# Performance work log

Hardware: AMD Instinct MI355X
Metric: run time of the kernel (lower is better)

Reference implementation:

```python
import jax, jax.numpy as jnp
import numpy as np

B, T, H, D = 4, 2048, 16, 128
ATTN = H * D
FREQ_BASE = 10000.0


def _rope(t, base):
    # t: [B, T, H, D]; ggml-style interleaved RoPE on pairs (2i, 2i+1)
    d = t.shape[-1]
    seq = t.shape[1]
    pos = jnp.arange(seq, dtype=jnp.float32)                      # [T]
    inv_freq = base ** (-jnp.arange(0, d, 2, dtype=jnp.float32) / d)  # [D/2]
    ang = pos[:, None] * inv_freq[None, :]                        # [T, D/2]
    cos = jnp.cos(ang)[None, :, None, :]                          # [1,T,1,D/2]
    sin = jnp.sin(ang)[None, :, None, :]
    t1 = t[..., 0::2]
    t2 = t[..., 1::2]
    r1 = t1 * cos - t2 * sin
    r2 = t1 * sin + t2 * cos
    return jnp.stack([r1, r2], axis=-1).reshape(t.shape)


def setup_inputs() -> dict:
    key = jax.random.key(0)
    ks = jax.random.split(key, 12)
    s = 1.0 / np.sqrt(ATTN)
    return {
        "x": jax.random.normal(ks[0], (B, T, ATTN), dtype=jnp.float32),
        "freqs_cos": jax.random.normal(ks[1], (T, D // 2), dtype=jnp.float32),
        "freqs_sin": jax.random.normal(ks[2], (T, D // 2), dtype=jnp.float32),
        "wq_w": jax.random.normal(ks[3], (ATTN, ATTN), dtype=jnp.float32) * s,
        "wq_b": jax.random.normal(ks[4], (ATTN,), dtype=jnp.float32) * s,
        "wk_w": jax.random.normal(ks[5], (ATTN, ATTN), dtype=jnp.float32) * s,
        "wk_b": jax.random.normal(ks[6], (ATTN,), dtype=jnp.float32) * s,
        "wv_w": jax.random.normal(ks[7], (ATTN, ATTN), dtype=jnp.float32) * s,
        "wv_b": jax.random.normal(ks[8], (ATTN,), dtype=jnp.float32) * s,
        "wo_w": jax.random.normal(ks[9], (ATTN, ATTN), dtype=jnp.float32) * s,
        "wo_b": jax.random.normal(ks[10], (ATTN,), dtype=jnp.float32) * s,
    }


def reference(x, freqs_cos, freqs_sin, wq_w, wq_b, wk_w, wk_b, wv_w, wv_b, wo_w, wo_b):
    # freqs_cos / freqs_sin accepted for signature compatibility but ignored
    b, t, _ = x.shape
    q = (x @ wq_w.T + wq_b).reshape(b, t, H, D)
    k = (x @ wk_w.T + wk_b).reshape(b, t, H, D)
    v = (x @ wv_w.T + wv_b).reshape(b, t, H, D)
    q = _rope(q, FREQ_BASE)
    k = _rope(k, FREQ_BASE)
    # causal SDPA over [B, H, T, D]
    scale = 1.0 / np.sqrt(D).astype(np.float32)
    scores = jnp.einsum("bqhd,bkhd->bhqk", q, k) * scale          # [B,H,T,T]
    mask = jnp.tril(jnp.ones((t, t), dtype=bool))
    scores = jnp.where(mask[None, None], scores, jnp.finfo(scores.dtype).min)
    probs = jax.nn.softmax(scores, axis=-1)
    y = jnp.einsum("bhqk,bkhd->bqhd", probs, v).reshape(b, t, H * D)
    return y @ wo_w.T + wo_b
```

## Files before the change

### kernel.cpp

```cpp
#include <hip/hip_runtime.h>
#include <math.h>

#define Tt 2048
#define Hh 16
#define Dd 128
#define ATTN 2048

typedef unsigned short u16;
typedef __attribute__((ext_vector_type(8))) short short8;
typedef __attribute__((ext_vector_type(4))) float f32x4;

__device__ __forceinline__ float bf2f(u16 h) {
    union { unsigned int u; float f; } x;
    x.u = ((unsigned int)h) << 16;
    return x.f;
}
__device__ __forceinline__ u16 f2bf(float f) {
    union { float f; unsigned int u; } x;
    x.f = f;
    unsigned int r = x.u + 0x7fffu + ((x.u >> 16) & 1u);
    return (u16)(r >> 16);
}
__device__ __forceinline__ void gl_lds16(const void* g, void* l) {
    __builtin_amdgcn_global_load_lds(
        (const __attribute__((address_space(1))) unsigned int*)g,
        (__attribute__((address_space(3))) unsigned int*)l, 16, 0, 0);
}

__global__ __launch_bounds__(256) void freq_kernel(float* __restrict__ cost,
                                                   float* __restrict__ sint) {
    int idx = blockIdx.x * 256 + threadIdx.x;
    if (idx >= Tt * 64) return;
    int t = idx >> 6, i = idx & 63;
    double inv = exp(-((double)(2 * i) / 128.0) * log(10000.0));
    double ang = (double)t * inv;
    cost[idx] = (float)cos(ang);
    sint[idx] = (float)sin(ang);
}

__global__ __launch_bounds__(256) void cvt_kernel(const float* __restrict__ in,
                                                  u16* __restrict__ out, int n4) {
    int i = blockIdx.x * 256 + threadIdx.x;
    if (i >= n4) return;
    float4 v = *(const float4*)(in + (size_t)i * 4);
    union { ushort4 u; u16 s[4]; } pk;
    pk.s[0] = f2bf(v.x); pk.s[1] = f2bf(v.y);
    pk.s[2] = f2bf(v.z); pk.s[3] = f2bf(v.w);
    *(ushort4*)(out + (size_t)i * 4) = pk.u;
}

template<int MODE>
__global__ __launch_bounds__(512, 2) void gemm_mfma(const u16* __restrict__ A,
                                                    const u16* __restrict__ W,
                                                    const float* __restrict__ bias,
                                                    void* __restrict__ Cout) {
    extern __shared__ u16 lds[];
    const int tid  = threadIdx.x;
    const int lane = tid & 63, w = tid >> 6;
    const int l15  = lane & 15, quad = lane >> 4;
    const int wm = w >> 2, wn = w & 3;

    const int id = blockIdx.x;
    const int bx = id & 7, by = id >> 3;
    const int m0 = by * 256, n0 = bx * 256;

    const f32x4 zero4 = {0.f, 0.f, 0.f, 0.f};
    f32x4 acc[8][4];
#pragma unroll
    for (int mt = 0; mt < 8; mt++)
#pragma unroll
        for (int nt = 0; nt < 4; nt++) acc[mt][nt] = zero4;

    const int srow = w * 16 + (lane >> 3);
    const int gsc  = ((lane & 7) ^ (lane >> 3)) * 8;
    const u16* Ag = A + (size_t)(m0 + srow) * 2048 + gsc;
    const u16* Wg = W + (size_t)(n0 + srow) * 2048 + gsc;
    const int wB = w * 1024;

    const int s7 = l15 & 7;
    const int cA = wm * 8192 + l15 * 64;
    const int cB = 16384 + (wn >> 1) * 8192 + ((wn & 1) * 64 + l15) * 64;
    const int ck0 = (quad ^ s7) * 8;
    const int ck1 = ((quad ^ s7) ^ 4) * 8;

#define STAGE(tt, dd, ss) do { \
    const u16* _g = (((ss) < 2) ? Ag : Wg) + (((ss) & 1) ? (size_t)(128 * 2048) : (size_t)0) \
                    + (size_t)(tt) * 64; \
    u16* _l = lds + (dd) * 32768 + (ss) * 8192 + wB; \
    gl_lds16(_g, _l); \
    gl_lds16(_g + (size_t)8 * 2048, _l + 512); \
} while (0)

    STAGE(0, 0, 0); STAGE(0, 0, 1); STAGE(0, 0, 2); STAGE(0, 0, 3);
    STAGE(1, 1, 0); STAGE(1, 1, 1);

    short8 af[4][2], bf[4][2];
    for (int t = 0; t < 32; t++) {
        const int d = t & 1, e = d ^ 1;
        const u16* bufd = lds + d * 32768;

        if (t < 31) { asm volatile("s_waitcnt vmcnt(4)" ::: "memory"); }
        else        { asm volatile("s_waitcnt vmcnt(0)" ::: "memory"); }
        __builtin_amdgcn_sched_barrier(0);
        __builtin_amdgcn_s_barrier();
        __builtin_amdgcn_sched_barrier(0);

#pragma unroll
        for (int mt = 0; mt < 4; mt++) {
            af[mt][0] = *(const short8*)(bufd + cA + mt * 1024 + ck0);
            af[mt][1] = *(const short8*)(bufd + cA + mt * 1024 + ck1);
        }
#pragma unroll
        for (int nt = 0; nt < 4; nt++) {
            bf[nt][0] = *(const short8*)(bufd + cB + nt * 1024 + ck0);
            bf[nt][1] = *(const short8*)(bufd + cB + nt * 1024 + ck1);
        }
        if (t + 1 < 32) STAGE(t + 1, e, 2);
        if (t + 1 < 32) STAGE(t + 1, e, 3);
        __builtin_amdgcn_s_setprio(1);
#pragma unroll
        for (int mt = 0; mt < 4; mt++)
#pragma unroll
            for (int nt = 0; nt < 4; nt++) {
                acc[mt][nt] = __builtin_amdgcn_mfma_f32_16x16x32_bf16(
                    af[mt][0], bf[nt][0], acc[mt][nt], 0, 0, 0);
                acc[mt][nt] = __builtin_amdgcn_mfma_f32_16x16x32_bf16(
                    af[mt][1], bf[nt][1], acc[mt][nt], 0, 0, 0);
            }
        __builtin_amdgcn_s_setprio(0);
#pragma unroll
        for (int mt = 0; mt < 4; mt++) {
            af[mt][0] = *(const short8*)(bufd + cA + (mt + 4) * 1024 + ck0);
            af[mt][1] = *(const short8*)(bufd + cA + (mt + 4) * 1024 + ck1);
        }
        asm volatile("s_waitcnt lgkmcnt(0)" ::: "memory");
        __builtin_amdgcn_sched_barrier(0);
        __builtin_amdgcn_s_barrier();
        __builtin_amdgcn_sched_barrier(0);
        if (t + 2 < 32) { STAGE(t + 2, d, 0); STAGE(t + 2, d, 1); }
        __builtin_amdgcn_s_setprio(1);
#pragma unroll
        for (int mt = 0; mt < 4; mt++)
#pragma unroll
            for (int nt = 0; nt < 4; nt++) {
                acc[mt + 4][nt] = __builtin_amdgcn_mfma_f32_16x16x32_bf16(
                    af[mt][0], bf[nt][0], acc[mt + 4][nt], 0, 0, 0);
                acc[mt + 4][nt] = __builtin_amdgcn_mfma_f32_16x16x32_bf16(
                    af[mt][1], bf[nt][1], acc[mt + 4][nt], 0, 0, 0);
            }
        __builtin_amdgcn_s_setprio(0);
    }
#undef STAGE

    float bn[4];
#pragma unroll
    for (int nt = 0; nt < 4; nt++) bn[nt] = bias[n0 + wn * 64 + nt * 16 + l15];

    if (MODE == 0) {
        float* C = (float*)Cout;
#pragma unroll
        for (int mt = 0; mt < 8; mt++) {
            int m = m0 + wm * 128 + mt * 16 + quad * 4;
#pragma unroll
            for (int nt = 0; nt < 4; nt++) {
                int n = n0 + wn * 64 + nt * 16 + l15;
#pragma unroll
                for (int r = 0; r < 4; r++)
                    C[(size_t)(m + r) * 2048 + n] = acc[mt][nt][r] + bn[nt];
            }
        }
    } else if (MODE == 1) {
        u16* C = (u16*)Cout;
#pragma unroll
        for (int mt = 0; mt < 8; mt++) {
            int m = m0 + wm * 128 + mt * 16 + quad * 4;
            int b = m >> 11, tr = m & 2047;
#pragma unroll
            for (int nt = 0; nt < 4; nt++) {
                int n = n0 + wn * 64 + nt * 16 + l15;
                int h = n >> 7, dd = n & 127;
                size_t base = ((size_t)(b * Hh + h) * Tt + tr) * Dd + dd;
#pragma unroll
                for (int r = 0; r < 4; r++)
                    C[base + (size_t)r * Dd] = f2bf(acc[mt][nt][r] + bn[nt]);
            }
        }
    } else {
        u16* C = (u16*)Cout;
        const int b = m0 >> 11;
#pragma unroll
        for (int mt = 0; mt < 8; mt++) {
            int tloc = (m0 & 2047) + wm * 128 + mt * 16 + quad * 4;
#pragma unroll
            for (int nt = 0; nt < 4; nt++) {
                int n = n0 + wn * 64 + nt * 16 + l15;
                int h = n >> 7, dd = n & 127;
                union { ushort4 u; u16 s[4]; } pk;
#pragma unroll
                for (int r = 0; r < 4; r++) pk.s[r] = f2bf(acc[mt][nt][r] + bn[nt]);
                *(ushort4*)&C[((size_t)(b * Hh + h) * Dd + dd) * Tt + tloc] = pk.u;
            }
        }
    }
}

#define QSCALE 0.12751743f
__global__ __launch_bounds__(256) void rope_kernel(u16* __restrict__ q,
                                                   u16* __restrict__ k,
                                                   const float* __restrict__ cost,
                                                   const float* __restrict__ sint) {
    int p = blockIdx.x * 256 + threadIdx.x;
    int g4 = (p & 15) * 4;
    int t  = (p >> 4) & 2047;
    float4 c4 = *(const float4*)(cost + t * 64 + g4);
    float4 s4 = *(const float4*)(sint + t * 64 + g4);
    float cc[4] = {c4.x, c4.y, c4.z, c4.w};
    float ss[4] = {s4.x, s4.y, s4.z, s4.w};
    size_t off = (size_t)p * 8;
    short8 qv = *(short8*)(q + off);
    short8 kv = *(short8*)(k + off);
    short8 qo, ko;
#pragma unroll
    for (int j = 0; j < 4; j++) {
        float q0 = bf2f((u16)qv[2 * j]), q1 = bf2f((u16)qv[2 * j + 1]);
        qo[2 * j]     = (short)f2bf((q0 * cc[j] - q1 * ss[j]) * QSCALE);
        qo[2 * j + 1] = (short)f2bf((q0 * ss[j] + q1 * cc[j]) * QSCALE);
        float k0 = bf2f((u16)kv[2 * j]), k1 = bf2f((u16)kv[2 * j + 1]);
        ko[2 * j]     = (short)f2bf(k0 * cc[j] - k1 * ss[j]);
        ko[2 * j + 1] = (short)f2bf(k0 * ss[j] + k1 * cc[j]);
    }
    *(short8*)(q + off) = qo;
    *(short8*)(k + off) = ko;
}

__global__ __launch_bounds__(256) void flash_mfma(const u16* __restrict__ Q,
                                                  const u16* __restrict__ K,
                                                  const u16* __restrict__ Vt,
                                                  u16* __restrict__ O) {
    __shared__ u16 Ks[64 * 128];
    __shared__ u16 Vs[128 * 64];
    __shared__ u16 Ps[4][32 * 72];
    __shared__ float als[4][32];
    __shared__ float lls[4][32];
    const int tid  = threadIdx.x;
    const int lane = tid & 63, w = tid >> 6;
    const int l15  = lane & 15, quad = lane >> 4;

    const int id  = blockIdx.x;
    const int bh  = (id & 7) * 8 + ((id >> 3) & 7);
    const int bxp = id >> 6;

    const u16* Kg[4]; const u16* Vg[4];
    u16* KsD[4]; u16* VsD[4];
#pragma unroll
    for (int cc = 0; cc < 4; cc++) {
        int kp = w * 16 + cc * 4 + quad;
        int gs = l15 ^ (cc * 4 + quad);
        Kg[cc]  = K + ((size_t)bh * Tt + kp) * Dd + gs * 8;
        KsD[cc] = Ks + (w * 4 + cc) * 512;
        int d  = w * 32 + cc * 8 + (lane >> 3);
        int gv = (lane & 7) ^ (lane >> 3);
        Vg[cc]  = Vt + ((size_t)bh * Dd + d) * Tt + gv * 8;
        VsD[cc] = Vs + (w * 4 + cc) * 512;
    }

    const f32x4 zero4 = {0.f, 0.f, 0.f, 0.f};

    for (int ph = 0; ph < 2; ph++) {
        const int qt = ph ? bxp : 15 - bxp;
        const int q0 = qt * 128;

        short8 qf[2][4];
        const u16* Qb = Q + ((size_t)bh * Tt + q0 + w * 32 + l15) * Dd + quad * 8;
#pragma unroll
        for (int nt = 0; nt < 2; nt++)
#pragma unroll
            for (int ks = 0; ks < 4; ks++)
                qf[nt][ks] = *(const short8*)(Qb + nt * 16 * Dd + ks * 32);

        f32x4 Oa[2][8];
#pragma unroll
        for (int mo = 0; mo < 2; mo++)
#pragma unroll
            for (int nt2 = 0; nt2 < 8; nt2++) Oa[mo][nt2] = zero4;
        float mrow[2] = {-INFINITY, -INFINITY};
        float lrow[2] = {0.f, 0.f};

        const int nkt = 2 * qt + 2;
        for (int kt = 0; kt < nkt; kt++) {
            __syncthreads();
#pragma unroll
            for (int cc = 0; cc < 4; cc++) gl_lds16(Kg[cc] + (size_t)kt * 64 * Dd, KsD[cc]);
#pragma unroll
            for (int cc = 0; cc < 4; cc++) gl_lds16(Vg[cc] + kt * 64, VsD[cc]);
            __syncthreads();

            if (kt * 64 > q0 + w * 32 + 31) continue;

            f32x4 sc[4][2];
#pragma unroll
            for (int mt = 0; mt < 4; mt++) { sc[mt][0] = zero4; sc[mt][1] = zero4; }
            __builtin_amdgcn_s_setprio(1);
#pragma unroll
            for (int ks = 0; ks < 4; ks++) {
                short8 kf[4];
#pragma unroll
                for (int mt = 0; mt < 4; mt++)
                    kf[mt] = *(const short8*)(Ks + (mt * 16 + l15) * 128 +
                                              (((ks * 4 + quad) ^ l15) * 8));
#pragma unroll
                for (int mt = 0; mt < 4; mt++) {
                    sc[mt][0] = __builtin_amdgcn_mfma_f32_16x16x32_bf16(kf[mt], qf[0][ks], sc[mt][0], 0, 0, 0);
                    sc[mt][1] = __builtin_amdgcn_mfma_f32_16x16x32_bf16(kf[mt], qf[1][ks], sc[mt][1], 0, 0, 0);
                }
            }
            __builtin_amdgcn_s_setprio(0);

            const bool diag = (kt * 64 + 63 > q0 + w * 32);
#pragma unroll
            for (int nt = 0; nt < 2; nt++) {
                const int q_g = q0 + w * 32 + nt * 16 + l15;
                float sv[16];
#pragma unroll
                for (int mt = 0; mt < 4; mt++)
#pragma unroll
                    for (int r = 0; r < 4; r++)
                        sv[mt * 4 + r] = sc[mt][nt][r];
                if (diag) {
#pragma unroll
                    for (int mt = 0; mt < 4; mt++)
#pragma unroll
                        for (int r = 0; r < 4; r++) {
                            int kp_g = kt * 64 + mt * 16 + quad * 4 + r;
                            if (kp_g > q_g) sv[mt * 4 + r] = -INFINITY;
                        }
                }
                float m8[8], m4[4];
#pragma unroll
                for (int e = 0; e < 8; e++) m8[e] = fmaxf(sv[e], sv[e + 8]);
#pragma unroll
                for (int e = 0; e < 4; e++) m4[e] = fmaxf(m8[e], m8[e + 4]);
                float mx = fmaxf(fmaxf(m4[0], m4[1]), fmaxf(m4[2], m4[3]));
                mx = fmaxf(mx, __shfl_xor(mx, 16, 64));
                mx = fmaxf(mx, __shfl_xor(mx, 32, 64));
                float mnew = fmaxf(mrow[nt], mx);
                mnew = (mnew - mrow[nt] <= 8.f) ? mrow[nt] : mnew;
                float alpha = exp2f(mrow[nt] - mnew);
                float pv[16];
#pragma unroll
                for (int e = 0; e < 16; e++) pv[e] = exp2f(sv[e] - mnew);
                float s8[8], s4[4];
#pragma unroll
                for (int e = 0; e < 8; e++) s8[e] = pv[e] + pv[e + 8];
#pragma unroll
                for (int e = 0; e < 4; e++) s4[e] = s8[e] + s8[e + 4];
                float rs = (s4[0] + s4[1]) + (s4[2] + s4[3]);
                rs += __shfl_xor(rs, 16, 64);
                rs += __shfl_xor(rs, 32, 64);
                lrow[nt] = lrow[nt] * alpha + rs;
                mrow[nt] = mnew;
                if (quad == 0) als[w][nt * 16 + l15] = alpha;
#pragma unroll
                for (int mt = 0; mt < 4; mt++) {
                    union { ushort4 u; u16 s[4]; } pk;
#pragma unroll
                    for (int r = 0; r < 4; r++) pk.s[r] = f2bf(pv[mt * 4 + r]);
                    *(ushort4*)&Ps[w][(nt * 16 + l15) * 72 + mt * 16 + quad * 4] = pk.u;
                }
            }

            float ao[2][4];
            bool need = false;
#pragma unroll
            for (int mo = 0; mo < 2; mo++)
#pragma unroll
                for (int r = 0; r < 4; r++) {
                    ao[mo][r] = als[w][mo * 16 + quad * 4 + r];
                    need |= (ao[mo][r] != 1.f);
                }
            if (__any(need)) {
#pragma unroll
                for (int mo = 0; mo < 2; mo++)
#pragma unroll
                    for (int nt2 = 0; nt2 < 8; nt2++)
#pragma unroll
                        for (int r = 0; r < 4; r++) Oa[mo][nt2][r] *= ao[mo][r];
            }

            __builtin_amdgcn_s_setprio(1);
#pragma unroll
            for (int ks2 = 0; ks2 < 2; ks2++) {
                short8 pf[2];
#pragma unroll
                for (int mo = 0; mo < 2; mo++)
                    pf[mo] = *(const short8*)&Ps[w][(mo * 16 + l15) * 72 + ks2 * 32 + quad * 8];
#pragma unroll
                for (int nt2 = 0; nt2 < 8; nt2++) {
                    short8 vf = *(const short8*)(Vs + (nt2 * 16 + l15) * 64 +
                                                 (((ks2 * 4 + quad) ^ (l15 & 7)) * 8));
                    Oa[0][nt2] = __builtin_amdgcn_mfma_f32_16x16x32_bf16(pf[0], vf, Oa[0][nt2], 0, 0, 0);
                    Oa[1][nt2] = __builtin_amdgcn_mfma_f32_16x16x32_bf16(pf[1], vf, Oa[1][nt2], 0, 0, 0);
                }
            }
            __builtin_amdgcn_s_setprio(0);
        }

        if (quad == 0) { lls[w][l15] = lrow[0]; lls[w][16 + l15] = lrow[1]; }
        float li[2][4];
#pragma unroll
        for (int mo = 0; mo < 2; mo++)
#pragma unroll
            for (int r = 0; r < 4; r++) li[mo][r] = 1.f / lls[w][mo * 16 + quad * 4 + r];
        const int b = bh >> 4, h = bh & 15;
#pragma unroll
        for (int mo = 0; mo < 2; mo++)
#pragma unroll
            for (int r = 0; r < 4; r++) {
                size_t ro = ((size_t)b * Tt + q0 + w * 32 + mo * 16 + quad * 4 + r) * ATTN
                            + h * Dd;
#pragma unroll
                for (int nt2 = 0; nt2 < 8; nt2++)
                    O[ro + nt2 * 16 + l15] = f2bf(Oa[mo][nt2][r] * li[mo][r]);
            }
    }
}

extern "C" void kernel_launch(void* const* d_in, const int* in_sizes, int n_in,
                              void* d_out, int out_size, void* d_ws, size_t ws_size,
                              hipStream_t stream) {
    const float* x    = (const float*)d_in[0];
    const float* wq_w = (const float*)d_in[3];
    const float* wq_b = (const float*)d_in[4];
    const float* wk_w = (const float*)d_in[5];
    const float* wk_b = (const float*)d_in[6];
    const float* wv_w = (const float*)d_in[7];
    const float* wv_b = (const float*)d_in[8];
    const float* wo_w = (const float*)d_in[9];
    const float* wo_b = (const float*)d_in[10];

    char* ws = (char*)d_ws;
    u16*   qb  = (u16*)(ws);
    u16*   kb  = (u16*)(ws + 33554432);
    u16*   vtb = (u16*)(ws + 67108864);
    u16*   xb  = (u16*)(ws + 100663296);
    u16*   obb = xb;
    u16*   wqb = (u16*)(ws + 134217728);
    u16*   wkb = (u16*)(ws + 142606336);
    u16*   wvb = (u16*)(ws + 150994944);
    u16*   wob = (u16*)(ws + 159383552);
    float* ct  = (float*)(ws + 167772160);
    float* st  = (float*)(ws + 168296448);

    freq_kernel<<<512, 256, 0, stream>>>(ct, st);
    cvt_kernel<<<16384, 256, 0, stream>>>(x, xb, 4194304);
    cvt_kernel<<<4096, 256, 0, stream>>>(wq_w, wqb, 1048576);
    cvt_kernel<<<4096, 256, 0, stream>>>(wk_w, wkb, 1048576);
    cvt_kernel<<<4096, 256, 0, stream>>>(wv_w, wvb, 1048576);
    cvt_kernel<<<4096, 256, 0, stream>>>(wo_w, wob, 1048576);

    gemm_mfma<1><<<256, 512, 131072, stream>>>(xb, wqb, wq_b, qb);
    gemm_mfma<1><<<256, 512, 131072, stream>>>(xb, wkb, wk_b, kb);
    gemm_mfma<2><<<256, 512, 131072, stream>>>(xb, wvb, wv_b, vtb);
    rope_kernel<<<8192, 256, 0, stream>>>(qb, kb, ct, st);
    flash_mfma<<<512, 256, 0, stream>>>(qb, kb, vtb, obb);
    gemm_mfma<0><<<256, 512, 131072, stream>>>(obb, wob, wo_b, (float*)d_out);
}
```

Before: 662.0 us.

## Restructure GEMM main loop into four barrier-separated half-K phases

Splits each K-tile iteration of the projection GEMM into four phases, each loading one half-K slice of A and B fragments, issuing one STAGE of the next tile, and running 16 MFMAs. It drops the two-tile-ahead prefetch of A and keeps only a one-tile lookahead with vmcnt(0) waits. The aim is lower register pressure (fewer live fragments) and interleaving of LDS reads, global-to-LDS loads and MFMAs. In exchange it adds many more s_barriers per iteration and reduces how far global loads run ahead, which risks exposed memory latency.

```diff
diff --git a/kernel.cpp b/kernel.cpp
--- a/kernel.cpp
+++ b/kernel.cpp
@@ -92,63 +92,102 @@
 } while (0)
 
     STAGE(0, 0, 0); STAGE(0, 0, 1); STAGE(0, 0, 2); STAGE(0, 0, 3);
-    STAGE(1, 1, 0); STAGE(1, 1, 1);
-
-    short8 af[4][2], bf[4][2];
+
+    short8 afQ[4], bfr[4][2];
     for (int t = 0; t < 32; t++) {
         const int d = t & 1, e = d ^ 1;
         const u16* bufd = lds + d * 32768;
-
-        if (t < 31) { asm volatile("s_waitcnt vmcnt(4)" ::: "memory"); }
-        else        { asm volatile("s_waitcnt vmcnt(0)" ::: "memory"); }
-        __builtin_amdgcn_sched_barrier(0);
-        __builtin_amdgcn_s_barrier();
-        __builtin_amdgcn_sched_barrier(0);
-
-#pragma unroll
-        for (int mt = 0; mt < 4; mt++) {
-            af[mt][0] = *(const short8*)(bufd + cA + mt * 1024 + ck0);
-            af[mt][1] = *(const short8*)(bufd + cA + mt * 1024 + ck1);
-        }
-#pragma unroll
-        for (int nt = 0; nt < 4; nt++) {
-            bf[nt][0] = *(const short8*)(bufd + cB + nt * 1024 + ck0);
-            bf[nt][1] = *(const short8*)(bufd + cB + nt * 1024 + ck1);
-        }
-        if (t + 1 < 32) STAGE(t + 1, e, 2);
-        if (t + 1 < 32) STAGE(t + 1, e, 3);
+        const bool pf = (t + 1 < 32);
+
+        asm volatile("s_waitcnt vmcnt(0)" ::: "memory");
+        __builtin_amdgcn_sched_barrier(0);
+        __builtin_amdgcn_s_barrier();
+        __builtin_amdgcn_sched_barrier(0);
+
+#pragma unroll
+        for (int i = 0; i < 4; i++)
+            afQ[i] = *(const short8*)(bufd + cA + i * 1024 + ck0);
+#pragma unroll
+        for (int i = 0; i < 4; i++)
+            bfr[i][0] = *(const short8*)(bufd + cB + i * 1024 + ck0);
+        if (pf) { STAGE(t + 1, e, 0); STAGE(t + 1, e, 1); }
+        __builtin_amdgcn_sched_barrier(0);
+        __builtin_amdgcn_s_barrier();
+        asm volatile("s_waitcnt lgkmcnt(0)" ::: "memory");
+        __builtin_amdgcn_sched_barrier(0);
         __builtin_amdgcn_s_setprio(1);
 #pragma unroll
-        for (int mt = 0; mt < 4; mt++)
-#pragma unroll
-            for (int nt = 0; nt < 4; nt++) {
-                acc[mt][nt] = __builtin_amdgcn_mfma_f32_16x16x32_bf16(
-                    af[mt][0], bf[nt][0], acc[mt][nt], 0, 0, 0);
-                acc[mt][nt] = __builtin_amdgcn_mfma_f32_16x16x32_bf16(
-                    af[mt][1], bf[nt][1], acc[mt][nt], 0, 0, 0);
-            }
+        for (int i = 0; i < 4; i++)
+#pragma unroll
+            for (int j = 0; j < 4; j++)
+                acc[i][j] = __builtin_amdgcn_mfma_f32_16x16x32_bf16(
+                    afQ[i], bfr[j][0], acc[i][j], 0, 0, 0);
         __builtin_amdgcn_s_setprio(0);
-#pragma unroll
-        for (int mt = 0; mt < 4; mt++) {
-            af[mt][0] = *(const short8*)(bufd + cA + (mt + 4) * 1024 + ck0);
-            af[mt][1] = *(const short8*)(bufd + cA + (mt + 4) * 1024 + ck1);
-        }
+        __builtin_amdgcn_sched_barrier(0);
+        __builtin_amdgcn_s_barrier();
+        __builtin_amdgcn_sched_barrier(0);
+
+#pragma unroll
+        for (int i = 0; i < 4; i++)
+            afQ[i] = *(const short8*)(bufd + cA + (i + 4) * 1024 + ck0);
+        if (pf) STAGE(t + 1, e, 2);
+        __builtin_amdgcn_sched_barrier(0);
+        __builtin_amdgcn_s_barrier();
         asm volatile("s_waitcnt lgkmcnt(0)" ::: "memory");
         __builtin_amdgcn_sched_barrier(0);
-        __builtin_amdgcn_s_barrier();
-        __builtin_amdgcn_sched_barrier(0);
-        if (t + 2 < 32) { STAGE(t + 2, d, 0); STAGE(t + 2, d, 1); }
         __builtin_amdgcn_s_setprio(1);
 #pragma unroll
-        for (int mt = 0; mt < 4; mt++)
-#pragma unroll
-            for (int nt = 0; nt < 4; nt++) {
-                acc[mt + 4][nt] = __builtin_amdgcn_mfma_f32_16x16x32_bf16(
-                    af[mt][0], bf[nt][0], acc[mt + 4][nt], 0, 0, 0);
-                acc[mt + 4][nt] = __builtin_amdgcn_mfma_f32_16x16x32_bf16(
-                    af[mt][1], bf[nt][1], acc[mt + 4][nt], 0, 0, 0);
-            }
+        for (int i = 0; i < 4; i++)
+#pragma unroll
+            for (int j = 0; j < 4; j++)
+                acc[i + 4][j] = __builtin_amdgcn_mfma_f32_16x16x32_bf16(
+                    afQ[i], bfr[j][0], acc[i + 4][j], 0, 0, 0);
         __builtin_amdgcn_s_setprio(0);
+        __builtin_amdgcn_sched_barrier(0);
+        __builtin_amdgcn_s_barrier();
+        __builtin_amdgcn_sched_barrier(0);
+
+#pragma unroll
+        for (int i = 0; i < 4; i++)
+            afQ[i] = *(const short8*)(bufd + cA + i * 1024 + ck1);
+#pragma unroll
+        for (int i = 0; i < 4; i++)
+            bfr[i][1] = *(const short8*)(bufd + cB + i * 1024 + ck1);
+        if (pf) STAGE(t + 1, e, 3);
+        __builtin_amdgcn_sched_barrier(0);
+        __builtin_amdgcn_s_barrier();
+        asm volatile("s_waitcnt lgkmcnt(0)" ::: "memory");
+        __builtin_amdgcn_sched_barrier(0);
+        __builtin_amdgcn_s_setprio(1);
+#pragma unroll
+        for (int i = 0; i < 4; i++)
+#pragma unroll
+            for (int j = 0; j < 4; j++)
+                acc[i][j] = __builtin_amdgcn_mfma_f32_16x16x32_bf16(
+                    afQ[i], bfr[j][1], acc[i][j], 0, 0, 0);
+        __builtin_amdgcn_s_setprio(0);
+        __builtin_amdgcn_sched_barrier(0);
+        __builtin_amdgcn_s_barrier();
+        __builtin_amdgcn_sched_barrier(0);
+
+#pragma unroll
+        for (int i = 0; i < 4; i++)
+            afQ[i] = *(const short8*)(bufd + cA + (i + 4) * 1024 + ck1);
+        __builtin_amdgcn_sched_barrier(0);
+        __builtin_amdgcn_s_barrier();
+        asm volatile("s_waitcnt lgkmcnt(0)" ::: "memory");
+        __builtin_amdgcn_sched_barrier(0);
+        __builtin_amdgcn_s_setprio(1);
+#pragma unroll
+        for (int i = 0; i < 4; i++)
+#pragma unroll
+            for (int j = 0; j < 4; j++)
+                acc[i + 4][j] = __builtin_amdgcn_mfma_f32_16x16x32_bf16(
+                    afQ[i], bfr[j][1], acc[i + 4][j], 0, 0, 0);
+        __builtin_amdgcn_s_setprio(0);
+        __builtin_amdgcn_sched_barrier(0);
+        __builtin_amdgcn_s_barrier();
+        __builtin_amdgcn_sched_barrier(0);
     }
 #undef STAGE
 
```

New measurement: 658.0 us. About the same (-0.6%).
